# Kernel tuning notes

Hardware: AMD Instinct MI355X
Metric: run time of the kernel (lower is better)

Reference implementation:

```python
import jax, jax.numpy as jnp
import numpy as np

D_MODEL = 1024
N_HEADS = 16
HEAD_DIM = D_MODEL // N_HEADS
SCALE = HEAD_DIM ** -0.5
MIN_VAL = jnp.finfo(jnp.float32).min


def setup_inputs() -> dict:
    key = jax.random.key(0)
    ks = jax.random.split(key, 7)
    B, T = 1, 2048
    s = D_MODEL ** -0.5
    return {
        "x": jax.random.normal(ks[0], (B, T, D_MODEL), dtype=jnp.float32),
        "Wq": jax.random.normal(ks[1], (D_MODEL, D_MODEL), dtype=jnp.float32) * s,
        "Wk1": jax.random.normal(ks[2], (D_MODEL, D_MODEL), dtype=jnp.float32) * s,
        "Wk2": jax.random.normal(ks[3], (D_MODEL, D_MODEL), dtype=jnp.float32) * s,
        "Wv": jax.random.normal(ks[4], (D_MODEL, D_MODEL), dtype=jnp.float32) * s,
        "Wo": jax.random.normal(ks[5], (D_MODEL, D_MODEL), dtype=jnp.float32) * s,
        "lambda_logit": jnp.zeros((N_HEADS,), dtype=jnp.float32),  # logit(0.5)=0
    }


def _split_heads(y):
    B, T, _ = y.shape
    return y.reshape(B, T, N_HEADS, HEAD_DIM).transpose(0, 2, 1, 3)  # [B,H,T,hd]


def reference(x, Wq, Wk1, Wk2, Wv, Wo, lambda_logit):
    B, T, _ = x.shape
    q = _split_heads(x @ Wq.T)
    k1 = _split_heads(x @ Wk1.T)
    k2 = _split_heads(x @ Wk2.T)
    v = _split_heads(x @ Wv.T)

    s1 = jnp.einsum("bhqd,bhkd->bhqk", q, k1) * SCALE
    s2 = jnp.einsum("bhqd,bhkd->bhqk", q, k2) * SCALE

    causal = jnp.arange(T)[None, :] <= jnp.arange(T)[:, None]  # [T,T] keep mask
    s1 = jnp.where(causal[None, None], s1, MIN_VAL)
    s2 = jnp.where(causal[None, None], s2, MIN_VAL)

    attn_exp = jax.nn.softmax(s1, axis=-1)
    attn_noise = jax.nn.softmax(s2, axis=-1)
    lam = jax.nn.sigmoid(lambda_logit)[None, :, None, None]
    attn = attn_exp - lam * attn_noise
    denom = jnp.maximum(jnp.sum(jnp.abs(attn), axis=-1, keepdims=True), 1e-6)
    attn = attn / denom

    out = jnp.einsum("bhqk,bhkd->bhqd", attn, v)
    out = out.transpose(0, 2, 1, 3).reshape(B, T, D_MODEL)
    return out @ Wo.T
```

## Files before the change

kernel.cpp:

```cpp
#include <hip/hip_runtime.h>

#define T_SEQ 2048
#define DM 1024
#define NH 16
#define HD 64
#define SC2 0.1803368801111731f
#define LS 72

typedef unsigned short u16;
typedef unsigned int u32;
typedef __attribute__((ext_vector_type(8))) short bf16x8;
typedef __attribute__((ext_vector_type(4))) float f32x4;

static __device__ __forceinline__ f32x4 mfma16(bf16x8 a, bf16x8 b, f32x4 c) {
    return __builtin_amdgcn_mfma_f32_16x16x32_bf16(a, b, c, 0, 0, 0);
}
static __device__ __forceinline__ float bf2f(u16 u) {
    union { u32 i; float f; } v; v.i = ((u32)u) << 16; return v.f;
}
static __device__ __forceinline__ u16 f2bf(float f) {
    union { float f; u32 i; } v; v.f = f;
    u32 x = v.i;
    x += 0x7FFFu + ((x >> 16) & 1u);
    return (u16)(x >> 16);
}
static __device__ __forceinline__ u16 f2bf_t(float f) {
    union { float f; u32 i; } v; v.f = f;
    return (u16)(v.i >> 16);
}
static __device__ __forceinline__ u32 pk2(float lo, float hi) {
    return (u32)f2bf(lo) | ((u32)f2bf(hi) << 16);
}
static __device__ __forceinline__ float qsum16(float v) {
#pragma unroll
    for (int o = 1; o < 16; o <<= 1) v += __shfl_xor(v, o, 64);
    return v;
}
static __device__ __forceinline__ float ex2(float x) {
    return __builtin_amdgcn_exp2f(x);
}

static __device__ __forceinline__ void gl16(const u16* g, u16* l) {
    __builtin_amdgcn_global_load_lds(
        (const __attribute__((address_space(1))) void*)g,
        (__attribute__((address_space(3))) void*)l,
        16, 0, 0);
}

template <int NISS>
static __device__ __forceinline__ void stage_async(const u16* src, size_t row0,
                                                   size_t lds_, size_t col0,
                                                   u16* dst, int tid) {
#pragma unroll
    for (int it = 0; it < NISS; it++) {
        int r = it * 32 + (tid >> 3);
        int cg = (tid & 7) ^ (r & 7);
        gl16(&src[(row0 + r) * lds_ + col0 + cg * 8], &dst[(it * 256 + tid) * 8]);
    }
}
static __device__ __forceinline__ bf16x8 frag(const u16* buf, int R, int co) {
    return *(const bf16x8*)(&buf[R * 64 + co]);
}

__global__ __launch_bounds__(256) void detect_dtype(const u16* __restrict__ x,
                                                    int* __restrict__ flag) {
    __shared__ int tot;
    const int tid = threadIdx.x;
    if (tid == 0) tot = 0;
    __syncthreads();
    int c = 0;
#pragma unroll
    for (int i = 0; i < 4; i++) {
        u16 v = x[2 * (tid * 4 + i)];
        int e = (v >> 7) & 0xFF;
        c += (e >= 110 && e <= 140) ? 1 : 0;
    }
    atomicAdd(&tot, c);
    __syncthreads();
    if (tid == 0) *flag = (tot >= 512) ? 1 : 0;
}

__global__ __launch_bounds__(256) void cvt_bf16(
    const int* __restrict__ flag,
    const float* __restrict__ x, const float* __restrict__ wq,
    const float* __restrict__ wk1, const float* __restrict__ wk2,
    const float* __restrict__ wv, const float* __restrict__ wo,
    u16* __restrict__ xc, u16* __restrict__ wqc, u16* __restrict__ wk1c,
    u16* __restrict__ wk2c, u16* __restrict__ wvc, u16* __restrict__ woc) {
    if (*flag) return;
    const int b = blockIdx.x;
    const int tid = threadIdx.x;
    const float* src;
    u16* dst;
    int rel;
    if (b < 1024)      { src = x;   dst = xc;   rel = b; }
    else if (b < 1536) { src = wq;  dst = wqc;  rel = b - 1024; }
    else if (b < 2048) { src = wk1; dst = wk1c; rel = b - 1536; }
    else if (b < 2560) { src = wk2; dst = wk2c; rel = b - 2048; }
    else if (b < 3072) { src = wv;  dst = wvc;  rel = b - 2560; }
    else               { src = wo;  dst = woc;  rel = b - 3072; }
    size_t idx = (size_t)rel * 2048 + (size_t)tid * 8;
    const float* s = src + idx;
    uint4 a = *(const uint4*)s;
    uint4 bq = *(const uint4*)(s + 4);
    const float* af = (const float*)&a;
    const float* bf = (const float*)&bq;
    uint4 r;
    r.x = pk2(af[0], af[1]); r.y = pk2(af[2], af[3]);
    r.z = pk2(bf[0], bf[1]); r.w = pk2(bf[2], bf[3]);
    *(uint4*)(dst + idx) = r;
}

__global__ __launch_bounds__(256) void qkv_gemm(
    const int* __restrict__ flag,
    const void* __restrict__ x0, const void* __restrict__ wq0,
    const void* __restrict__ wk10, const void* __restrict__ wk20,
    const void* __restrict__ wv0,
    const u16* __restrict__ xc, const u16* __restrict__ wqc,
    const u16* __restrict__ wk1c, const u16* __restrict__ wk2c,
    const u16* __restrict__ wvc,
    u16* __restrict__ qd, u16* __restrict__ k1d, u16* __restrict__ k2d,
    u16* __restrict__ vtd) {
    __shared__ __align__(16) u16 As[2][128 * 64];
    __shared__ __align__(16) u16 Bs[2][128 * 64];

    const int f = *flag;
    const int tid = threadIdx.x;
    const int w = blockIdx.x >> 3;
    const int n0 = (blockIdx.x & 7) * 128;
    const int m0 = blockIdx.y * 128;
    const u16* xb = f ? (const u16*)x0 : xc;
    const u16* Bb;
    if (w == 0)      Bb = f ? (const u16*)wq0  : wqc;
    else if (w == 1) Bb = f ? (const u16*)wk10 : wk1c;
    else if (w == 2) Bb = f ? (const u16*)wk20 : wk2c;
    else             Bb = f ? (const u16*)wv0  : wvc;

    const int lane = tid & 63, wave = tid >> 6;
    const int lr = lane & 15, quad = lane >> 4;
    const int wm = (wave >> 1) * 64, wn = (wave & 1) * 64;
    const int sw = lr & 7;

    f32x4 acc[4][4];
#pragma unroll
    for (int i = 0; i < 4; i++)
#pragma unroll
        for (int j = 0; j < 4; j++) acc[i][j] = (f32x4){0.f, 0.f, 0.f, 0.f};

    stage_async<4>(xb, m0, DM, 0, As[0], tid);
    stage_async<4>(Bb, n0, DM, 0, Bs[0], tid);
    for (int k0 = 0; k0 < DM; k0 += 64) {
        const int cur = (k0 >> 6) & 1;
        __syncthreads();
        if (k0 + 64 < DM) {
            stage_async<4>(xb, m0, DM, k0 + 64, As[cur ^ 1], tid);
            stage_async<4>(Bb, n0, DM, k0 + 64, Bs[cur ^ 1], tid);
        }
#pragma unroll
        for (int kk = 0; kk < 2; kk++) {
            const int co = ((kk * 4 + quad) ^ sw) * 8;
            bf16x8 af[4], bfr[4];
#pragma unroll
            for (int i = 0; i < 4; i++) af[i] = frag(As[cur], wm + i * 16 + lr, co);
#pragma unroll
            for (int j = 0; j < 4; j++) bfr[j] = frag(Bs[cur], wn + j * 16 + lr, co);
#pragma unroll
            for (int i = 0; i < 4; i++)
#pragma unroll
                for (int j = 0; j < 4; j++) acc[i][j] = mfma16(af[i], bfr[j], acc[i][j]);
        }
    }

#pragma unroll
    for (int i = 0; i < 4; i++)
#pragma unroll
        for (int j = 0; j < 4; j++)
#pragma unroll
            for (int r = 0; r < 4; r++) {
                int t = m0 + wm + i * 16 + quad * 4 + r;
                int o = n0 + wn + j * 16 + lr;
                float val = acc[i][j][r];
                if (w == 0) val *= SC2;
                u16 vbits = f2bf(val);
                int hh = o >> 6, d0 = o & 63;
                if (w == 3)
                    vtd[((size_t)hh * HD + d0) * T_SEQ + t] = vbits;
                else
                    ((w == 0) ? qd : (w == 1) ? k1d : k2d)[((size_t)hh * T_SEQ + t) * HD + d0] = vbits;
            }
}

#define ATTN_MAP()                                            \
    const int b = blockIdx.x;                                 \
    const int par = b >> 9;                                   \
    const int rem = b & 511;                                  \
    const int h = rem & 15;                                   \
    const int bi = rem >> 4;                                  \
    const int qt = (bi < 16) ? bi : 47 - bi;                  \
    const int t0 = qt * 64;                                   \
    const int tid = threadIdx.x;                              \
    const int lane = tid & 63, wave = tid >> 6;               \
    const int lr = lane & 15, quad = lane >> 4;               \
    const int wm = wave * 16;                                 \
    const int sw = lr & 7;

__global__ __launch_bounds__(256) void attn_a(
    const u16* __restrict__ qg, const u16* __restrict__ k1g,
    const u16* __restrict__ k2g, float* __restrict__ zp) {
    __shared__ __align__(16) u16 k1s[64 * 64];
    __shared__ __align__(16) u16 k2s[64 * 64];
    ATTN_MAP();

    const u16* qh = qg + (size_t)h * T_SEQ * HD;
    const u16* k1h = k1g + (size_t)h * T_SEQ * HD;
    const u16* k2h = k2g + (size_t)h * T_SEQ * HD;

    bf16x8 aq[2];
#pragma unroll
    for (int kk = 0; kk < 2; kk++)
        aq[kk] = *(const bf16x8*)(&qh[(size_t)(t0 + wm + lr) * HD + kk * 32 + quad * 8]);

    float z1a[4] = {0.f, 0.f, 0.f, 0.f}, z2a[4] = {0.f, 0.f, 0.f, 0.f};

    for (int kt = par; kt <= qt; kt += 4) {
        __syncthreads();
        stage_async<2>(k1h, (size_t)kt * 64, HD, 0, k1s, tid);
        stage_async<2>(k2h, (size_t)kt * 64, HD, 0, k2s, tid);
        __syncthreads();

        f32x4 sa[4], sb[4];
#pragma unroll
        for (int j = 0; j < 4; j++) { sa[j] = (f32x4){0.f,0.f,0.f,0.f}; sb[j] = (f32x4){0.f,0.f,0.f,0.f}; }
#pragma unroll
        for (int kk = 0; kk < 2; kk++) {
            const int co = ((kk * 4 + quad) ^ sw) * 8;
#pragma unroll
            for (int j = 0; j < 4; j++) {
                sa[j] = mfma16(aq[kk], frag(k1s, j * 16 + lr, co), sa[j]);
                sb[j] = mfma16(aq[kk], frag(k2s, j * 16 + lr, co), sb[j]);
            }
        }

        if (kt < qt) {
#pragma unroll
            for (int r = 0; r < 4; r++)
#pragma unroll
                for (int j = 0; j < 4; j++) {
                    z1a[r] += ex2(sa[j][r]);
                    z2a[r] += ex2(sb[j][r]);
                }
        } else {
#pragma unroll
            for (int r = 0; r < 4; r++) {
                const int grow = t0 + wm + quad * 4 + r;
#pragma unroll
                for (int j = 0; j < 4; j++) {
                    int gcol = kt * 64 + j * 16 + lr;
                    if (gcol <= grow) {
                        z1a[r] += ex2(sa[j][r]);
                        z2a[r] += ex2(sb[j][r]);
                    }
                }
            }
        }
    }

#pragma unroll
    for (int r = 0; r < 4; r++) {
        float s1 = qsum16(z1a[r]);
        float s2 = qsum16(z2a[r]);
        if (lr == 0) {
            int row = t0 + wm + quad * 4 + r;
            zp[((size_t)(par * 2 + 0) * NH + h) * T_SEQ + row] = s1;
            zp[((size_t)(par * 2 + 1) * NH + h) * T_SEQ + row] = s2;
        }
    }
}

__global__ __launch_bounds__(256) void attn_b(
    const u16* __restrict__ qg, const u16* __restrict__ k1g,
    const u16* __restrict__ k2g, const u16* __restrict__ vtg,
    const float* __restrict__ zp, const void* __restrict__ lamsrc,
    const int* __restrict__ flag,
    float* __restrict__ dpart, u16* __restrict__ opart) {
    __shared__ __align__(16) u16 k1s[64 * 64];
    __shared__ __align__(16) u16 k2s[64 * 64];
    __shared__ __align__(16) u16 ps[4][16 * LS];
    ATTN_MAP();

    const int f = *flag;
    float lamlogit = f ? bf2f(((const u16*)lamsrc)[h]) : ((const float*)lamsrc)[h];
    const float lam = 1.0f / (1.0f + __expf(-lamlogit));

    const u16* qh = qg + (size_t)h * T_SEQ * HD;
    const u16* k1h = k1g + (size_t)h * T_SEQ * HD;
    const u16* k2h = k2g + (size_t)h * T_SEQ * HD;
    const u16* vh = vtg + (size_t)h * HD * T_SEQ;

    bf16x8 aq[2];
#pragma unroll
    for (int kk = 0; kk < 2; kk++)
        aq[kk] = *(const bf16x8*)(&qh[(size_t)(t0 + wm + lr) * HD + kk * 32 + quad * 8]);

    float z1l[4], z2l[4];
#pragma unroll
    for (int r = 0; r < 4; r++) {
        int row = t0 + wm + quad * 4 + r;
        float z1 = 0.f, z2 = 0.f;
#pragma unroll
        for (int p = 0; p < 4; p++) {
            z1 += zp[((size_t)(p * 2 + 0) * NH + h) * T_SEQ + row];
            z2 += zp[((size_t)(p * 2 + 1) * NH + h) * T_SEQ + row];
        }
        z1l[r] = -__log2f(z1);
        z2l[r] = __log2f(lam) - __log2f(z2);
    }

    f32x4 oac[4];
#pragma unroll
    for (int j = 0; j < 4; j++) oac[j] = (f32x4){0.f, 0.f, 0.f, 0.f};
    float dacc[4] = {0.f, 0.f, 0.f, 0.f};

    for (int kt = par; kt <= qt; kt += 2) {
        __syncthreads();
        stage_async<2>(k1h, (size_t)kt * 64, HD, 0, k1s, tid);
        stage_async<2>(k2h, (size_t)kt * 64, HD, 0, k2s, tid);
        bf16x8 vfr[2][4];
#pragma unroll
        for (int kk = 0; kk < 2; kk++)
#pragma unroll
            for (int j = 0; j < 4; j++)
                vfr[kk][j] = *(const bf16x8*)(
                    &vh[(size_t)(j * 16 + lr) * T_SEQ + kt * 64 + (kk * 4 + quad) * 8]);
        __syncthreads();

        f32x4 sa[4], sb[4];
#pragma unroll
        for (int j = 0; j < 4; j++) { sa[j] = (f32x4){0.f,0.f,0.f,0.f}; sb[j] = (f32x4){0.f,0.f,0.f,0.f}; }
#pragma unroll
        for (int kk = 0; kk < 2; kk++) {
            const int co = ((kk * 4 + quad) ^ sw) * 8;
#pragma unroll
            for (int j = 0; j < 4; j++) {
                sa[j] = mfma16(aq[kk], frag(k1s, j * 16 + lr, co), sa[j]);
                sb[j] = mfma16(aq[kk], frag(k2s, j * 16 + lr, co), sb[j]);
            }
        }

        if (kt < qt) {
#pragma unroll
            for (int r = 0; r < 4; r++)
#pragma unroll
                for (int j = 0; j < 4; j++) {
                    float p = ex2(sa[j][r] + z1l[r]) - ex2(sb[j][r] + z2l[r]);
                    dacc[r] += fabsf(p);
                    ps[wave][(quad * 4 + r) * LS + j * 16 + lr] = f2bf_t(p);
                }
        } else {
#pragma unroll
            for (int r = 0; r < 4; r++) {
                const int grow = t0 + wm + quad * 4 + r;
#pragma unroll
                for (int j = 0; j < 4; j++) {
                    int gcol = kt * 64 + j * 16 + lr;
                    float p = 0.f;
                    if (gcol <= grow)
                        p = ex2(sa[j][r] + z1l[r]) - ex2(sb[j][r] + z2l[r]);
                    dacc[r] += fabsf(p);
                    ps[wave][(quad * 4 + r) * LS + j * 16 + lr] = f2bf_t(p);
                }
            }
        }

#pragma unroll
        for (int kk = 0; kk < 2; kk++) {
            bf16x8 pa = *(const bf16x8*)(&ps[wave][lr * LS + kk * 32 + quad * 8]);
#pragma unroll
            for (int j = 0; j < 4; j++)
                oac[j] = mfma16(pa, vfr[kk][j], oac[j]);
        }
    }

#pragma unroll
    for (int r = 0; r < 4; r++) {
        float ds = qsum16(dacc[r]);
        if (lr == 0) {
            int row = t0 + wm + quad * 4 + r;
            dpart[((size_t)par * NH + h) * T_SEQ + row] = ds;
        }
    }
#pragma unroll
    for (int j = 0; j < 4; j++)
#pragma unroll
        for (int r = 0; r < 4; r++) {
            int row = t0 + wm + quad * 4 + r;
            opart[(size_t)par * T_SEQ * DM + (size_t)row * DM + h * HD + j * 16 + lr] =
                f2bf(oac[j][r]);
        }
}

__global__ __launch_bounds__(256) void normalize_o(
    const u16* __restrict__ opart, const float* __restrict__ dpart,
    u16* __restrict__ ao) {
    int g = blockIdx.x * 256 + threadIdx.x;
    int t = g >> 7;
    int cc = g & 127;
    int d0 = cc * 8;
    int h = d0 >> 6;
    float dsum = dpart[(size_t)h * T_SEQ + t] + dpart[(size_t)(NH + h) * T_SEQ + t];
    float rs = 1.f / fmaxf(dsum, 1e-6f);
    uint4 a = *(const uint4*)(&opart[(size_t)t * DM + d0]);
    uint4 bqq = *(const uint4*)(&opart[(size_t)T_SEQ * DM + (size_t)t * DM + d0]);
    const u32* au = (const u32*)&a;
    const u32* bu = (const u32*)&bqq;
    uint4 out;
    u32* ou = (u32*)&out;
#pragma unroll
    for (int i = 0; i < 4; i++) {
        float lo = (bf2f((u16)(au[i] & 0xFFFF)) + bf2f((u16)(bu[i] & 0xFFFF))) * rs;
        float hi = (bf2f((u16)(au[i] >> 16)) + bf2f((u16)(bu[i] >> 16))) * rs;
        ou[i] = pk2(lo, hi);
    }
    *(uint4*)(&ao[(size_t)t * DM + d0]) = out;
}

__global__ __launch_bounds__(256) void out_gemm(
    const u16* __restrict__ ab, const void* __restrict__ wo0,
    const u16* __restrict__ woc, const int* __restrict__ flag,
    void* __restrict__ outp) {
    __shared__ __align__(16) u16 As[2][64 * 64];
    __shared__ __align__(16) u16 Bs[2][64 * 64];

    const int f = *flag;
    const u16* wb = f ? (const u16*)wo0 : woc;
    const int n0 = blockIdx.x * 64;
    const int m0 = blockIdx.y * 64;
    const int tid = threadIdx.x;
    const int lane = tid & 63, wave = tid >> 6;
    const int lr = lane & 15, quad = lane >> 4;
    const int wm = (wave >> 1) * 32, wn = (wave & 1) * 32;
    const int sw = lr & 7;

    f32x4 acc[2][2];
#pragma unroll
    for (int i = 0; i < 2; i++)
#pragma unroll
        for (int j = 0; j < 2; j++) acc[i][j] = (f32x4){0.f, 0.f, 0.f, 0.f};

    stage_async<2>(ab, m0, DM, 0, As[0], tid);
    stage_async<2>(wb, n0, DM, 0, Bs[0], tid);
    for (int k0 = 0; k0 < DM; k0 += 64) {
        const int cur = (k0 >> 6) & 1;
        __syncthreads();
        if (k0 + 64 < DM) {
            stage_async<2>(ab, m0, DM, k0 + 64, As[cur ^ 1], tid);
            stage_async<2>(wb, n0, DM, k0 + 64, Bs[cur ^ 1], tid);
        }
#pragma unroll
        for (int kk = 0; kk < 2; kk++) {
            const int co = ((kk * 4 + quad) ^ sw) * 8;
            bf16x8 af[2], bfr[2];
#pragma unroll
            for (int i = 0; i < 2; i++) af[i] = frag(As[cur], wm + i * 16 + lr, co);
#pragma unroll
            for (int j = 0; j < 2; j++) bfr[j] = frag(Bs[cur], wn + j * 16 + lr, co);
#pragma unroll
            for (int i = 0; i < 2; i++)
#pragma unroll
                for (int j = 0; j < 2; j++) acc[i][j] = mfma16(af[i], bfr[j], acc[i][j]);
        }
    }

#pragma unroll
    for (int i = 0; i < 2; i++)
#pragma unroll
        for (int j = 0; j < 2; j++)
#pragma unroll
            for (int r = 0; r < 4; r++) {
                int t = m0 + wm + i * 16 + quad * 4 + r;
                int o = n0 + wn + j * 16 + lr;
                float val = acc[i][j][r];
                if (f)
                    ((u16*)outp)[(size_t)t * DM + o] = f2bf(val);
                else
                    ((float*)outp)[(size_t)t * DM + o] = val;
            }
}

extern "C" void kernel_launch(void* const* d_in, const int* in_sizes, int n_in,
                              void* d_out, int out_size, void* d_ws, size_t ws_size,
                              hipStream_t stream) {
    char* ws = (char*)d_ws;
    int* flag = (int*)(ws + 0);
    float* zp    = (float*)(ws + ((size_t)1 << 20));
    float* dpart = (float*)(ws + ((size_t)2 << 20));
    u16* qd  = (u16*)(ws + ((size_t)16 << 20));
    u16* k1d = (u16*)(ws + ((size_t)20 << 20));
    u16* k2d = (u16*)(ws + ((size_t)24 << 20));
    u16* vtd = (u16*)(ws + ((size_t)28 << 20));
    u16* ao  = (u16*)(ws + ((size_t)32 << 20));
    u16* opart = (u16*)(ws + ((size_t)36 << 20));
    u16* xc   = (u16*)(ws + ((size_t)44 << 20));
    u16* wqc  = (u16*)(ws + ((size_t)48 << 20));
    u16* wk1c = (u16*)(ws + ((size_t)50 << 20));
    u16* wk2c = (u16*)(ws + ((size_t)52 << 20));
    u16* wvc  = (u16*)(ws + ((size_t)54 << 20));
    u16* woc  = (u16*)(ws + ((size_t)56 << 20));

    detect_dtype<<<dim3(1), 256, 0, stream>>>((const u16*)d_in[0], flag);
    cvt_bf16<<<dim3(3584), 256, 0, stream>>>(
        flag, (const float*)d_in[0], (const float*)d_in[1], (const float*)d_in[2],
        (const float*)d_in[3], (const float*)d_in[4], (const float*)d_in[5],
        xc, wqc, wk1c, wk2c, wvc, woc);
    qkv_gemm<<<dim3(32, 16), 256, 0, stream>>>(
        flag, d_in[0], d_in[1], d_in[2], d_in[3], d_in[4],
        xc, wqc, wk1c, wk2c, wvc, qd, k1d, k2d, vtd);
    attn_a<<<dim3(2048), 256, 0, stream>>>(qd, k1d, k2d, zp);
    attn_b<<<dim3(1024), 256, 0, stream>>>(qd, k1d, k2d, vtd, zp, d_in[6], flag,
                                           dpart, opart);
    normalize_o<<<dim3(1024), 256, 0, stream>>>(opart, dpart, ao);
    out_gemm<<<dim3(16, 32), 256, 0, stream>>>(ao, d_in[5], woc, flag, d_out);
}
```

Before: 209.5 us.

## Double-buffer K tiles in attention and swizzle the P scratch layout

The attention kernel now keeps two LDS buffers for the K1 and K2 tiles. The next key tile is prefetched asynchronously while the current one is used for the QK MFMAs, and one of the two barriers per iteration is dropped. Separately, the per-wave P scratch buffer no longer uses a padded stride; it uses a 64-wide row with an XOR swizzle on 8-element chunks to avoid LDS bank conflicts. The cost is more LDS per block, which could lower occupancy. Correctness also depends on the async loads having completed before the single remaining barrier.

Result: no change. 205.9 us (-1.7%).

```diff
diff --git a/kernel.cpp b/kernel.cpp
--- a/kernel.cpp
+++ b/kernel.cpp
@@ -5,7 +5,6 @@
 #define NH 16
 #define HD 64
 #define SC2 0.1803368801111731f
-#define LS 72
 
 typedef unsigned short u16;
 typedef unsigned int u32;
@@ -283,9 +282,9 @@
     const float* __restrict__ zp, const void* __restrict__ lamsrc,
     const int* __restrict__ flag,
     float* __restrict__ dpart, u16* __restrict__ opart) {
-    __shared__ __align__(16) u16 k1s[64 * 64];
-    __shared__ __align__(16) u16 k2s[64 * 64];
-    __shared__ __align__(16) u16 ps[4][16 * LS];
+    __shared__ __align__(16) u16 k1s[2][64 * 64];
+    __shared__ __align__(16) u16 k2s[2][64 * 64];
+    __shared__ __align__(16) u16 ps[4][16 * 64];
     ATTN_MAP();
 
     const int f = *flag;
@@ -321,10 +320,14 @@
     for (int j = 0; j < 4; j++) oac[j] = (f32x4){0.f, 0.f, 0.f, 0.f};
     float dacc[4] = {0.f, 0.f, 0.f, 0.f};
 
+    const int prow_base = quad * 4;
+
+    stage_async<2>(k1h, (size_t)par * 64, HD, 0, k1s[0], tid);
+    stage_async<2>(k2h, (size_t)par * 64, HD, 0, k2s[0], tid);
+    int cur = 0;
     for (int kt = par; kt <= qt; kt += 2) {
         __syncthreads();
-        stage_async<2>(k1h, (size_t)kt * 64, HD, 0, k1s, tid);
-        stage_async<2>(k2h, (size_t)kt * 64, HD, 0, k2s, tid);
+
         bf16x8 vfr[2][4];
 #pragma unroll
         for (int kk = 0; kk < 2; kk++)
@@ -332,7 +335,11 @@
             for (int j = 0; j < 4; j++)
                 vfr[kk][j] = *(const bf16x8*)(
                     &vh[(size_t)(j * 16 + lr) * T_SEQ + kt * 64 + (kk * 4 + quad) * 8]);
-        __syncthreads();
+
+        if (kt + 2 <= qt) {
+            stage_async<2>(k1h, (size_t)(kt + 2) * 64, HD, 0, k1s[cur ^ 1], tid);
+            stage_async<2>(k2h, (size_t)(kt + 2) * 64, HD, 0, k2s[cur ^ 1], tid);
+        }
 
         f32x4 sa[4], sb[4];
 #pragma unroll
@@ -342,23 +349,28 @@
             const int co = ((kk * 4 + quad) ^ sw) * 8;
 #pragma unroll
             for (int j = 0; j < 4; j++) {
-                sa[j] = mfma16(aq[kk], frag(k1s, j * 16 + lr, co), sa[j]);
-                sb[j] = mfma16(aq[kk], frag(k2s, j * 16 + lr, co), sb[j]);
+                sa[j] = mfma16(aq[kk], frag(k1s[cur], j * 16 + lr, co), sa[j]);
+                sb[j] = mfma16(aq[kk], frag(k2s[cur], j * 16 + lr, co), sb[j]);
             }
         }
 
         if (kt < qt) {
 #pragma unroll
-            for (int r = 0; r < 4; r++)
+            for (int r = 0; r < 4; r++) {
+                const int prow = prow_base + r;
 #pragma unroll
                 for (int j = 0; j < 4; j++) {
                     float p = ex2(sa[j][r] + z1l[r]) - ex2(sb[j][r] + z2l[r]);
                     dacc[r] += fabsf(p);
-                    ps[wave][(quad * 4 + r) * LS + j * 16 + lr] = f2bf_t(p);
+                    int chunk = j * 2 + (lr >> 3);
+                    int scol = ((chunk ^ (prow & 7)) << 3) | (lr & 7);
+                    ps[wave][prow * 64 + scol] = f2bf_t(p);
                 }
+            }
         } else {
 #pragma unroll
             for (int r = 0; r < 4; r++) {
+                const int prow = prow_base + r;
                 const int grow = t0 + wm + quad * 4 + r;
 #pragma unroll
                 for (int j = 0; j < 4; j++) {
@@ -367,18 +379,22 @@
                     if (gcol <= grow)
                         p = ex2(sa[j][r] + z1l[r]) - ex2(sb[j][r] + z2l[r]);
                     dacc[r] += fabsf(p);
-                    ps[wave][(quad * 4 + r) * LS + j * 16 + lr] = f2bf_t(p);
+                    int chunk = j * 2 + (lr >> 3);
+                    int scol = ((chunk ^ (prow & 7)) << 3) | (lr & 7);
+                    ps[wave][prow * 64 + scol] = f2bf_t(p);
                 }
             }
         }
 
 #pragma unroll
         for (int kk = 0; kk < 2; kk++) {
-            bf16x8 pa = *(const bf16x8*)(&ps[wave][lr * LS + kk * 32 + quad * 8]);
+            int schunk = (kk * 4 + quad) ^ (lr & 7);
+            bf16x8 pa = *(const bf16x8*)(&ps[wave][lr * 64 + schunk * 8]);
 #pragma unroll
             for (int j = 0; j < 4; j++)
                 oac[j] = mfma16(pa, vfr[kk][j], oac[j]);
         }
+        cur ^= 1;
     }
 
 #pragma unroll
```
